# Optimization experiments

Hardware: AMD Instinct MI355X
Metric: run time of the kernel (lower is better)

The kernel has to match this reference:

```python
import jax, jax.numpy as jnp
import numpy as np


def _to_complex(x):
    # trailing axis holds (real, imag)
    return x[..., 0] + 1j * x[..., 1]


def _nufft2c(img, omega, csm):
    """Exact type-2 non-uniform DFT with coil sensitivities (reference for nufft2c_torch).

    img:   (H, W) real or complex image
    omega: (2, M) k-space coords in cycles/pixel, in [-0.5, 0.5]
    csm:   (C, H, W) complex coil sensitivity maps
    returns (C, M) complex k-space, centered & orthonormal-style 1/sqrt(HW) scaling.
    """
    H, W = img.shape
    y = jnp.arange(H, dtype=jnp.float32) - H / 2.0  # centered pixel coords
    z = jnp.arange(W, dtype=jnp.float32) - W / 2.0
    ey = jnp.exp(-2j * jnp.pi * omega[0][:, None] * y[None, :])  # (M, H)
    ez = jnp.exp(-2j * jnp.pi * omega[1][:, None] * z[None, :])  # (M, W)
    sim = csm * img[None, :, :].astype(csm.dtype)                # (C, H, W)
    tmp = jnp.einsum('chw,mw->cmh', sim, ez)                     # (C, M, H)
    k = jnp.einsum('cmh,mh->cm', tmp, ey) / np.float32(np.sqrt(H * W))
    return k


def setup_inputs() -> dict:
    key = jax.random.key(0)
    k0, k1, k2, k3, k4 = jax.random.split(key, 5)
    H = W = 300
    C = 4       # coils
    M = 4096    # non-Cartesian k-space samples
    img_pred = jax.random.normal(k0, (H, W, 1), jnp.float32)
    kdata = jax.random.normal(k1, (1, C, M, 2), jnp.float32)
    all_omega = jax.random.uniform(k2, (1, 2, M), jnp.float32) - 0.5  # cycles/pixel
    all_dcomp = jax.random.uniform(k3, (1, M), jnp.float32)
    all_csm = jax.random.normal(k4, (C, H, W, 2), jnp.float32)
    return {
        'img_pred': img_pred,
        'kdata': kdata,
        'all_omega': all_omega,
        'all_dcomp': all_dcomp,
        'all_csm': all_csm,
    }


def reference(img_pred, kdata, all_omega, all_dcomp, all_csm):
    Ncontrast = 1
    csm = _to_complex(all_csm)   # (C, H, W)
    kd = _to_complex(kdata)      # (Ncontrast, C, M)
    two_pi = jnp.float32(2.0 * np.pi)
    # radial k-space weighting, (Ncontrast, M)
    weight = jnp.sqrt((all_omega[:, 0, :] * two_pi) ** 2 +
                      (all_omega[:, 1, :] * two_pi) ** 2) + 1.0
    loss = jnp.float32(0.0)
    for ii in range(Ncontrast):
        img = img_pred[:, :, ii]                       # (H, W)
        ksp = _nufft2c(img, all_omega[ii], csm)        # (C, M)
        d = weight[ii][None, :] * (ksp - kd[ii])       # weighted complex residual
        # MSELoss over view_as_real == mean over all real & imag components
        loss = loss + jnp.mean(jnp.stack([d.real, d.imag]) ** 2)
    return loss
```

## Files before the change

kernel.cpp:

```cpp
#include <hip/hip_runtime.h>
#include <math.h>

#define HH 300
#define WW 300
#define CC 4
#define MM 4096
#define KP 640
#define NKC (KP/32)
#define CSTRIDE 384
#define MP (CC*CSTRIDE)
#define NP 8192
#define NRB (MP/128)

typedef __attribute__((ext_vector_type(4))) float f32x4;
typedef __attribute__((ext_vector_type(4))) int int4v;
typedef __attribute__((ext_vector_type(8))) int int8v;

#define TWO_PI 6.283185307179586f

__device__ __forceinline__ size_t cmaddr(int R, int row, int k) {
    return ((size_t)(k >> 5) * R + row) * 32 + (k & 31);
}

__device__ __forceinline__ float aval(const float* img, const float* csm,
                                      int c, int h, int k) {
    if (k >= 2 * WW) return 0.0f;
    int w = (k < WW) ? k : k - WW;
    float im = img[h * WW + w];
    const float* cs = csm + (((size_t)c * HH + h) * WW + w) * 2;
    return ((k < WW) ? cs[0] : cs[1]) * im;
}

__global__ __launch_bounds__(256) void prep_kernel(
    const float* __restrict__ img, const float* __restrict__ csm,
    const float* __restrict__ omega, unsigned char* __restrict__ A,
    unsigned char* __restrict__ B, float* __restrict__ out)
{
    const int bid = blockIdx.x;
    if (bid == 0 && threadIdx.x == 0) out[0] = 0.0f;
    const int ABLK = (MP * KP / 2) / 256;
    if (bid < ABLK) {
        int idx = bid * 256 + threadIdx.x;
        int row = idx / (KP / 2);
        int k   = (idx - row * (KP / 2)) * 2;
        int c = row / CSTRIDE;
        int h = row - c * CSTRIDE;
        float v0 = 0.0f, v1 = 0.0f;
        if (h < HH) { v0 = aval(img, csm, c, h, k); v1 = aval(img, csm, c, h, k + 1); }
        int pk = __builtin_amdgcn_cvt_pk_fp8_f32(v0, v1, 0, false);
        *(ushort*)(A + cmaddr(MP, row, k)) = (ushort)pk;
    } else {
        int idx = (bid - ABLK) * 256 + threadIdx.x;
        int m  = idx / 160;
        int wp = idx - m * 160;
        if (wp < 150) {
            int w = wp * 2;
            float om1 = omega[MM + m];
            float s0, c0, s1, c1;
            __sincosf(TWO_PI * om1 * (float)(w - 150), &s0, &c0);
            __sincosf(TWO_PI * om1 * (float)(w - 149), &s1, &c1);
            ushort rr = (ushort)__builtin_amdgcn_cvt_pk_fp8_f32(c0, c1, 0, false);
            ushort ii = (ushort)__builtin_amdgcn_cvt_pk_fp8_f32(-s0, -s1, 0, false);
            ushort ni = (ushort)__builtin_amdgcn_cvt_pk_fp8_f32(s0, s1, 0, false);
            *(ushort*)(B + cmaddr(NP, m,      w))        = rr;
            *(ushort*)(B + cmaddr(NP, m,      WW + w))   = ni;
            *(ushort*)(B + cmaddr(NP, m + MM, w))        = ii;
            *(ushort*)(B + cmaddr(NP, m + MM, WW + w))   = rr;
        } else {
            int k = 600 + (wp - 150) * 4;
            *(unsigned int*)(B + cmaddr(NP, m,      k)) = 0u;
            *(unsigned int*)(B + cmaddr(NP, m + MM, k)) = 0u;
        }
    }
}

__global__ __launch_bounds__(256) void gemm_kernel(
    const unsigned char* __restrict__ A, const unsigned char* __restrict__ B,
    const float* __restrict__ omega, float2* __restrict__ P)
{
    __shared__ float2 red[128];

    const int t    = threadIdx.x;
    const int wave = t >> 6;
    const int ln   = t & 63;
    const int row0 = blockIdx.y * 128;
    const int col0 = blockIdx.x * 128;
    const int wr = wave >> 1, wc = wave & 1;
    const int lr = ln & 15;
    const int lq = ln >> 4;

    if (t < 128) red[t] = make_float2(0.0f, 0.0f);

    const int arow = row0 + wr * 64 + lr;
    const int bcol = col0 + wc * 64 + lr;

    f32x4 acc[4][4] = {};

    #pragma unroll
    for (int kc = 0; kc < NKC; kc += 4) {
        int8v a[4], b[4];
        #pragma unroll
        for (int i = 0; i < 4; ++i) {
            const unsigned char* pA = A + ((size_t)(kc + lq) * MP + arow + i * 16) * 32;
            int4v lo = *(const int4v*)pA;
            int4v hi = *(const int4v*)(pA + 16);
            a[i] = __builtin_shufflevector(lo, hi, 0, 1, 2, 3, 4, 5, 6, 7);
        }
        #pragma unroll
        for (int j = 0; j < 4; ++j) {
            const unsigned char* pB = B + ((size_t)(kc + lq) * NP + bcol + j * 16) * 32;
            int4v lo = *(const int4v*)pB;
            int4v hi = *(const int4v*)(pB + 16);
            b[j] = __builtin_shufflevector(lo, hi, 0, 1, 2, 3, 4, 5, 6, 7);
        }
        #pragma unroll
        for (int i = 0; i < 4; ++i)
            #pragma unroll
            for (int j = 0; j < 4; ++j)
                acc[i][j] = __builtin_amdgcn_mfma_scale_f32_16x16x128_f8f6f4(
                    a[i], b[j], acc[i][j], 0, 0,
                    0, 0x7f7f7f7f, 0, 0x7f7f7f7f);
    }

    __syncthreads();

    const int c  = row0 / CSTRIDE;
    const int h0 = row0 - c * CSTRIDE;

    #pragma unroll
    for (int j = 0; j < 4; ++j) {
        const int jcol = wc * 64 + j * 16 + lr;
        const int m = (col0 + jcol) & (MM - 1);
        const float om0 = omega[m];
        float ss, sc;
        __sincosf(TWO_PI * om0, &ss, &sc);
        const float str = sc, sti = -ss;
        float s2r = str * str - sti * sti, s2i = 2.0f * str * sti;
        float s4r = s2r * s2r - s2i * s2i, s4i = 2.0f * s2r * s2i;
        float s8r = s4r * s4r - s4i * s4i, s8i = 2.0f * s4r * s4i;
        float s16r = s8r * s8r - s8i * s8i, s16i = 2.0f * s8r * s8i;

        const int hb0 = h0 + wr * 64 + lq * 4;
        float sn, cs;
        __sincosf(TWO_PI * om0 * (float)(hb0 - 150), &sn, &cs);
        float byr = cs, byi = -sn;

        float pr = 0.0f, pi = 0.0f;
        #pragma unroll
        for (int i = 0; i < 4; ++i) {
            float er = byr, ei = byi;
            #pragma unroll
            for (int r = 0; r < 4; ++r) {
                const float v = acc[i][j][r];
                pr = fmaf(v, er, pr);
                pi = fmaf(v, ei, pi);
                float nr = er * str - ei * sti;
                ei = er * sti + ei * str;
                er = nr;
            }
            float nbr = byr * s16r - byi * s16i;
            byi = byr * s16i + byi * s16r;
            byr = nbr;
        }
        pr += __shfl_down(pr, 32); pi += __shfl_down(pi, 32);
        pr += __shfl_down(pr, 16); pi += __shfl_down(pi, 16);
        if (lq == 0) {
            atomicAdd(&red[jcol].x, pr);
            atomicAdd(&red[jcol].y, pi);
        }
    }
    __syncthreads();

    if (t < 128) {
        const int rb = row0 >> 7;
        P[(size_t)rb * NP + col0 + t] = red[t];
    }
}

__global__ __launch_bounds__(64) void loss_kernel(
    const float2* __restrict__ P, const float* __restrict__ kdata,
    const float* __restrict__ omega, float* __restrict__ out)
{
    const int t = blockIdx.x * 64 + threadIdx.x;
    const int c = t >> 12;
    const int m = t & (MM - 1);

    float kr = 0.0f, ki = 0.0f;
    #pragma unroll
    for (int q = 0; q < 3; ++q) {
        const int rb = 3 * c + q;
        float2 p0 = P[(size_t)rb * NP + m];
        float2 p1 = P[(size_t)rb * NP + m + MM];
        kr += p0.x - p1.y;
        ki += p0.y + p1.x;
    }
    kr *= (1.0f / 300.0f);
    ki *= (1.0f / 300.0f);

    const float om0 = omega[m];
    const float om1 = omega[MM + m];
    const size_t kidx = ((size_t)c * MM + m) * 2;
    const float kdr = kdata[kidx];
    const float kdi = kdata[kidx + 1];
    const float w0 = om0 * TWO_PI, w1 = om1 * TWO_PI;
    const float wg = sqrtf(w0 * w0 + w1 * w1) + 1.0f;
    const float dr = wg * (kr - kdr);
    const float di = wg * (ki - kdi);
    float val = (dr * dr + di * di) * (1.0f / (2.0f * CC * MM));

    #pragma unroll
    for (int off = 32; off > 0; off >>= 1) val += __shfl_down(val, off);
    if (threadIdx.x == 0) atomicAdd(out, val);
}

extern "C" void kernel_launch(void* const* d_in, const int* in_sizes, int n_in,
                              void* d_out, int out_size, void* d_ws, size_t ws_size,
                              hipStream_t stream) {
    const float* img   = (const float*)d_in[0];
    const float* kdata = (const float*)d_in[1];
    const float* omega = (const float*)d_in[2];
    const float* csm   = (const float*)d_in[4];
    float* out = (float*)d_out;

    unsigned char* Aws = (unsigned char*)d_ws;
    unsigned char* Bws = (unsigned char*)d_ws + (1u << 20);
    float2*        Pws = (float2*)((char*)d_ws + (8u << 20));

    const int ablk = (MP * KP / 2) / 256;
    const int bblk = (MM * 160) / 256;
    prep_kernel<<<ablk + bblk, 256, 0, stream>>>(img, csm, omega, Aws, Bws, out);
    gemm_kernel<<<dim3(NP / 128, MP / 128), 256, 0, stream>>>(Aws, Bws, omega, Pws);
    loss_kernel<<<CC * MM / 64, 64, 0, stream>>>(Pws, kdata, omega, out);
}
```

Measured before the change: 84.35 us.

## Fuse loss reduction into GEMM epilogue with last-block counters and XCD-aware tiling

```diff
diff --git a/kernel.cpp b/kernel.cpp
--- a/kernel.cpp
+++ b/kernel.cpp
@@ -12,6 +12,10 @@
 #define NP 8192
 #define NRB (MP/128)
 
+#define ABLK 1920
+#define BBLK 2560
+#define ZBLK 129
+
 typedef __attribute__((ext_vector_type(4))) float f32x4;
 typedef __attribute__((ext_vector_type(4))) int int4v;
 typedef __attribute__((ext_vector_type(8))) int int8v;
@@ -34,11 +38,11 @@
 __global__ __launch_bounds__(256) void prep_kernel(
     const float* __restrict__ img, const float* __restrict__ csm,
     const float* __restrict__ omega, unsigned char* __restrict__ A,
-    unsigned char* __restrict__ B, float* __restrict__ out)
+    unsigned char* __restrict__ B, float* __restrict__ Kz,
+    int* __restrict__ counters, float* __restrict__ out)
 {
     const int bid = blockIdx.x;
     if (bid == 0 && threadIdx.x == 0) out[0] = 0.0f;
-    const int ABLK = (MP * KP / 2) / 256;
     if (bid < ABLK) {
         int idx = bid * 256 + threadIdx.x;
         int row = idx / (KP / 2);
@@ -49,7 +53,7 @@
         if (h < HH) { v0 = aval(img, csm, c, h, k); v1 = aval(img, csm, c, h, k + 1); }
         int pk = __builtin_amdgcn_cvt_pk_fp8_f32(v0, v1, 0, false);
         *(ushort*)(A + cmaddr(MP, row, k)) = (ushort)pk;
-    } else {
+    } else if (bid < ABLK + BBLK) {
         int idx = (bid - ABLK) * 256 + threadIdx.x;
         int m  = idx / 160;
         int wp = idx - m * 160;
@@ -71,20 +75,35 @@
             *(unsigned int*)(B + cmaddr(NP, m,      k)) = 0u;
             *(unsigned int*)(B + cmaddr(NP, m + MM, k)) = 0u;
         }
+    } else {
+        int idx = (bid - ABLK - BBLK) * 256 + threadIdx.x;
+        if (idx < 2 * CC * MM)          Kz[idx] = 0.0f;
+        else if (idx < 2 * CC * MM + 32) counters[idx - 2 * CC * MM] = 0;
     }
 }
 
 __global__ __launch_bounds__(256) void gemm_kernel(
     const unsigned char* __restrict__ A, const unsigned char* __restrict__ B,
-    const float* __restrict__ omega, float2* __restrict__ P)
+    const float* __restrict__ omega, const float* __restrict__ kdata,
+    float* __restrict__ Kacc, int* __restrict__ counters,
+    float* __restrict__ out)
 {
     __shared__ float2 red[128];
+    __shared__ int winner;
+    __shared__ float lred[4];
 
     const int t    = threadIdx.x;
     const int wave = t >> 6;
     const int ln   = t & 63;
-    const int row0 = blockIdx.y * 128;
-    const int col0 = blockIdx.x * 128;
+
+    const int flat = blockIdx.x;
+    const int xcd  = flat & 7;
+    const int q    = flat >> 3;
+    const int cb   = xcd * 8 + (q & 7);
+    const int rowb = q >> 3;
+    const int row0 = rowb * 128;
+    const int col0 = cb * 128;
+
     const int wr = wave >> 1, wc = wave & 1;
     const int lr = ln & 15;
     const int lq = ln >> 4;
@@ -171,46 +190,53 @@
     }
     __syncthreads();
 
+    const int g = (col0 >> 7) & 31;
+    const bool realcol = (col0 < MM);
     if (t < 128) {
-        const int rb = row0 >> 7;
-        P[(size_t)rb * NP + col0 + t] = red[t];
-    }
-}
-
-__global__ __launch_bounds__(64) void loss_kernel(
-    const float2* __restrict__ P, const float* __restrict__ kdata,
-    const float* __restrict__ omega, float* __restrict__ out)
-{
-    const int t = blockIdx.x * 64 + threadIdx.x;
-    const int c = t >> 12;
-    const int m = t & (MM - 1);
-
-    float kr = 0.0f, ki = 0.0f;
-    #pragma unroll
-    for (int q = 0; q < 3; ++q) {
-        const int rb = 3 * c + q;
-        float2 p0 = P[(size_t)rb * NP + m];
-        float2 p1 = P[(size_t)rb * NP + m + MM];
-        kr += p0.x - p1.y;
-        ki += p0.y + p1.x;
-    }
-    kr *= (1.0f / 300.0f);
-    ki *= (1.0f / 300.0f);
-
-    const float om0 = omega[m];
-    const float om1 = omega[MM + m];
-    const size_t kidx = ((size_t)c * MM + m) * 2;
-    const float kdr = kdata[kidx];
-    const float kdi = kdata[kidx + 1];
-    const float w0 = om0 * TWO_PI, w1 = om1 * TWO_PI;
-    const float wg = sqrtf(w0 * w0 + w1 * w1) + 1.0f;
-    const float dr = wg * (kr - kdr);
-    const float di = wg * (ki - kdi);
-    float val = (dr * dr + di * di) * (1.0f / (2.0f * CC * MM));
-
-    #pragma unroll
-    for (int off = 32; off > 0; off >>= 1) val += __shfl_down(val, off);
-    if (threadIdx.x == 0) atomicAdd(out, val);
+        const float2 p = red[t];
+        const int m = (col0 + t) & (MM - 1);
+        float* kc = Kacc + ((size_t)c * MM + m) * 2;
+        if (realcol) {
+            atomicAdd(kc,     p.x);
+            atomicAdd(kc + 1, p.y);
+        } else {
+            atomicAdd(kc,    -p.y);
+            atomicAdd(kc + 1,  p.x);
+        }
+    }
+    __threadfence();
+    __syncthreads();
+    if (t == 0) winner = (atomicAdd(&counters[g], 1) == 23) ? 1 : 0;
+    __syncthreads();
+
+    if (winner) {
+        __threadfence();
+        float val = 0.0f;
+        #pragma unroll
+        for (int u = 0; u < 2; ++u) {
+            const int idx = u * 256 + t;
+            const int c2 = idx >> 7;
+            const int m  = g * 128 + (idx & 127);
+            float* kc = Kacc + ((size_t)c2 * MM + m) * 2;
+            float kr = atomicAdd(kc,     0.0f) * (1.0f / 300.0f);
+            float ki = atomicAdd(kc + 1, 0.0f) * (1.0f / 300.0f);
+            const float om0 = omega[m];
+            const float om1 = omega[MM + m];
+            const size_t kidx = ((size_t)c2 * MM + m) * 2;
+            const float kdr = kdata[kidx];
+            const float kdi = kdata[kidx + 1];
+            const float w0 = om0 * TWO_PI, w1 = om1 * TWO_PI;
+            const float wg = sqrtf(w0 * w0 + w1 * w1) + 1.0f;
+            const float dr = wg * (kr - kdr);
+            const float di = wg * (ki - kdi);
+            val += (dr * dr + di * di) * (1.0f / (2.0f * CC * MM));
+        }
+        #pragma unroll
+        for (int off = 32; off > 0; off >>= 1) val += __shfl_down(val, off);
+        if (ln == 0) lred[wave] = val;
+        __syncthreads();
+        if (t == 0) atomicAdd(out, lred[0] + lred[1] + lred[2] + lred[3]);
+    }
 }
 
 extern "C" void kernel_launch(void* const* d_in, const int* in_sizes, int n_in,
@@ -224,11 +250,11 @@
 
     unsigned char* Aws = (unsigned char*)d_ws;
     unsigned char* Bws = (unsigned char*)d_ws + (1u << 20);
-    float2*        Pws = (float2*)((char*)d_ws + (8u << 20));
-
-    const int ablk = (MP * KP / 2) / 256;
-    const int bblk = (MM * 160) / 256;
-    prep_kernel<<<ablk + bblk, 256, 0, stream>>>(img, csm, omega, Aws, Bws, out);
-    gemm_kernel<<<dim3(NP / 128, MP / 128), 256, 0, stream>>>(Aws, Bws, omega, Pws);
-    loss_kernel<<<CC * MM / 64, 64, 0, stream>>>(Pws, kdata, omega, out);
-}
+    float* Kacc    = (float*)((char*)d_ws + (8u << 20));
+    int*   counters = (int*)((char*)d_ws + (8u << 20) + (256u << 10));
+
+    prep_kernel<<<ABLK + BBLK + ZBLK, 256, 0, stream>>>(
+        img, csm, omega, Aws, Bws, Kacc, counters, out);
+    gemm_kernel<<<NP / 128 * (MP / 128), 256, 0, stream>>>(
+        Aws, Bws, omega, kdata, Kacc, counters, out);
+}
```

After: 132.0 us. 1.56x slower.
